# Performance work log

Measured on AMD Instinct MI355X. Metric: run time of the kernel, lower is better.

The kernel has to match this reference:

```python
import jax, jax.numpy as jnp
import numpy as np

B = 16384
WIDE_DIM = 256          # 32 wide features * dim 8
DEEP_DIM = 1024         # 64 deep features * embedding_dim 16
SHARED = [2048, 1024, 512]
DOMAIN = [512, 256]
NUM_DOMAINS = 8


def setup_inputs() -> dict:
    key = jax.random.key(0)
    ks = jax.random.split(key, 20)
    s = 0.01  # embedding_init_var-style small init
    inp = {
        "wide_features": jax.random.normal(ks[0], (B, WIDE_DIM), jnp.float32),
        "deep_features": jax.random.normal(ks[1], (B, DEEP_DIM), jnp.float32),
        "domain_ids": jax.random.randint(ks[2], (B,), 0, NUM_DOMAINS, jnp.int64),
        # shared MLP (weights stored [in, out])
        "W1": jax.random.normal(ks[3], (DEEP_DIM, SHARED[0]), jnp.float32) * s,
        "b1": jnp.zeros((SHARED[0],), jnp.float32),
        "W2": jax.random.normal(ks[4], (SHARED[0], SHARED[1]), jnp.float32) * s,
        "b2": jnp.zeros((SHARED[1],), jnp.float32),
        "W3": jax.random.normal(ks[5], (SHARED[1], SHARED[2]), jnp.float32) * s,
        "b3": jnp.zeros((SHARED[2],), jnp.float32),
        # domain-specific MLP
        "Wd1": jax.random.normal(ks[6], (SHARED[2], DOMAIN[0]), jnp.float32) * s,
        "bd1": jnp.zeros((DOMAIN[0],), jnp.float32),
        "Wd2": jax.random.normal(ks[7], (DOMAIN[0], DOMAIN[1]), jnp.float32) * s,
        "bd2": jnp.zeros((DOMAIN[1],), jnp.float32),
        # per-domain output heads: Linear(DOMAIN[-1], 1) per domain
        "Wh": jax.random.normal(ks[8], (NUM_DOMAINS, DOMAIN[1]), jnp.float32) * s,
        "bh": jnp.zeros((NUM_DOMAINS,), jnp.float32),
    }
    return inp


def reference(wide_features, deep_features, domain_ids,
              W1, b1, W2, b2, W3, b3, Wd1, bd1, Wd2, bd2, Wh, bh):
    # wide part: sum embedding output to a scalar logit per sample [B, 1]
    wide = jnp.sum(wide_features, axis=1, keepdims=True)
    # shared deep MLP
    h = jax.nn.relu(deep_features @ W1 + b1)
    h = jax.nn.relu(h @ W2 + b2)
    shared = jax.nn.relu(h @ W3 + b3)          # [B, 512]
    # domain-specific tower (shared across domains)
    d = jax.nn.relu(shared @ Wd1 + bd1)
    d = jax.nn.relu(d @ Wd2 + bd2)             # [B, 256]
    # per-sample domain head routing: gather head weights, fused dot
    w = Wh[domain_ids]                          # [B, 256]
    head = jnp.sum(d * w, axis=1, keepdims=True) + bh[domain_ids][:, None]  # [B, 1]
    out = jax.nn.sigmoid(wide + head)
    return (out, shared, d)
```

## Files before the change

### kernel.cpp

```cpp
#include <hip/hip_runtime.h>
#include <hip/hip_bf16.h>


typedef __attribute__((ext_vector_type(8))) short short8;
typedef __attribute__((ext_vector_type(4))) float f32x4;

static __device__ __forceinline__ unsigned short f2bf_bits(float x) {
  __hip_bfloat16 h = __float2bfloat16(x);
  return __builtin_bit_cast(unsigned short, h);
}
static __device__ __forceinline__ float bf_bits2f(unsigned short u) {
  __hip_bfloat16 h = __builtin_bit_cast(__hip_bfloat16, u);
  return __bfloat162float(h);
}

static __device__ __forceinline__ void gload16(const void* g, void* l) {
  __builtin_amdgcn_global_load_lds(
      (const __attribute__((address_space(1))) void*)g,
      (__attribute__((address_space(3))) void*)l, 16, 0, 0);
}

static __device__ __forceinline__ unsigned lds_u32(const void* p) {
  return (unsigned)(uintptr_t)(const __attribute__((address_space(3))) void*)p;
}

static __device__ __forceinline__ short8 dsr(unsigned addr) {
  short8 r;
  asm volatile("ds_read_b128 %0, %1" : "=v"(r) : "v"(addr));
  return r;
}

#define MFMA16(a, b, c) __builtin_amdgcn_mfma_f32_16x16x32_bf16((a), (b), (c), 0, 0, 0)
#define SB0() __builtin_amdgcn_sched_barrier(0)
#define PRIO(x) __builtin_amdgcn_s_setprio(x)
#define BAR() __builtin_amdgcn_s_barrier()
#define MEMFENCE() asm volatile("" ::: "memory")

__global__ void transpose_convert(const float* __restrict__ W,
                                  __hip_bfloat16* __restrict__ Wt,
                                  int K, int N) {
  __shared__ float tile[64][65];
  const int k0 = blockIdx.y * 64;
  const int n0 = blockIdx.x * 64;
  const int t  = threadIdx.x;
  const int tn = t & 63;
  const int t4 = t >> 6;
#pragma unroll
  for (int p = 0; p < 16; ++p) {
    int kl = p * 4 + t4;
    tile[kl][tn] = W[(size_t)(k0 + kl) * N + (n0 + tn)];
  }
  __syncthreads();
#pragma unroll
  for (int p = 0; p < 16; ++p) {
    int nl = p * 4 + t4;
    Wt[(size_t)(n0 + nl) * K + (k0 + tn)] = __float2bfloat16(tile[tn][nl]);
  }
}

__global__ void f32_to_bf16(const float* __restrict__ in,
                            unsigned short* __restrict__ out, int n8) {
  int i = blockIdx.x * blockDim.x + threadIdx.x;
  if (i >= n8) return;
  const f32x4* p = (const f32x4*)in + (size_t)i * 2;
  f32x4 a = p[0], b = p[1];
  short8 o;
  o[0] = (short)f2bf_bits(a[0]); o[1] = (short)f2bf_bits(a[1]);
  o[2] = (short)f2bf_bits(a[2]); o[3] = (short)f2bf_bits(a[3]);
  o[4] = (short)f2bf_bits(b[0]); o[5] = (short)f2bf_bits(b[1]);
  o[6] = (short)f2bf_bits(b[2]); o[7] = (short)f2bf_bits(b[3]);
  *(short8*)(out + (size_t)i * 8) = o;
}

__global__ __launch_bounds__(512, 2) void gemm_2c(
    const __hip_bfloat16* __restrict__ A,
    const __hip_bfloat16* __restrict__ Bt,
    const float* __restrict__ bias,
    __hip_bfloat16* __restrict__ Cb,
    float* __restrict__ Cf,
    int N, int K, int nbx) {
  __shared__ char lds[131072];

  const int tid  = threadIdx.x;
  const int lane = tid & 63;
  const int wid  = tid >> 6;
  const int wm   = wid >> 2;
  const int wn   = wid & 3;

  const int nwg = gridDim.x;
  const int cpx = nwg >> 3;
  const int id  = blockIdx.x;
  const int swz = (id & 7) * cpx + (id >> 3);
  const int bm  = (swz / nbx) * 256;
  const int bn  = (swz % nbx) * 256;

  const int ln15 = lane & 15;
  const unsigned cswz = (unsigned)((((lane >> 4) ^ (lane & 7)) << 4));

  const unsigned aoff = (unsigned)((wm * 128 + ln15) * 128) + cswz;
  const unsigned boff = 32768u + (unsigned)((wn * 64 + ln15) * 128) + cswz;

  const int nt = K >> 6;

  const __hip_bfloat16* baseA = A  + (size_t)(bm + (tid >> 3)) * K +
                                ((tid & 7) ^ ((tid >> 3) & 7)) * 8;
  const __hip_bfloat16* baseB = Bt + (size_t)(bn + (tid >> 3)) * K +
                                ((tid & 7) ^ ((tid >> 3) & 7)) * 8;
  const unsigned ldst0 = (unsigned)(wid * 1024);

  auto stage = [&](int kt, int half, int isB) {
    const __hip_bfloat16* base = isB ? baseB : baseA;
    char* dst = lds + ((kt & 1) * 65536) + (isB ? 32768 : 0) + half * 16384;
#pragma unroll
    for (int q = 0; q < 2; ++q) {
      gload16(base + (size_t)((half * 128 + q * 64) * K + kt * 64),
              dst + q * 8192 + ldst0);
    }
  };

  auto LD = [&](unsigned off) -> short8 {
    return *(const short8*)&lds[off];
  };

  f32x4 acc[8][4] = {};
  short8 aLo[4][2], aHi[4][2], b0v[2][2], b1v[2][2];

  stage(0, 0, 1); stage(0, 1, 1); stage(0, 0, 0); stage(0, 1, 0);
  if (nt > 1) {
    stage(1, 0, 1); stage(1, 1, 1); stage(1, 0, 0); stage(1, 1, 0);
    asm volatile("s_waitcnt vmcnt(8)");
  } else {
    asm volatile("s_waitcnt vmcnt(0)");
  }
  BAR();
  MEMFENCE();
#pragma unroll
  for (int mi = 0; mi < 4; ++mi)
#pragma unroll
    for (int kk = 0; kk < 2; ++kk)
      aLo[mi][kk] = LD((aoff + (unsigned)(mi * 2048)) ^ (unsigned)(kk << 6));
#pragma unroll
  for (int nj = 0; nj < 2; ++nj)
#pragma unroll
    for (int kk = 0; kk < 2; ++kk)
      b0v[nj][kk] = LD((boff + (unsigned)(nj * 2048)) ^ (unsigned)(kk << 6));

  for (int t = 0; t < nt; ++t) {
    const unsigned po = (unsigned)(t & 1) * 65536u;
    const unsigned pn = po ^ 65536u;

#pragma unroll
    for (int nj = 0; nj < 2; ++nj)
#pragma unroll
      for (int kk = 0; kk < 2; ++kk)
        b1v[nj][kk] = LD((po + boff + (unsigned)((nj + 2) * 2048)) ^ (unsigned)(kk << 6));
    PRIO(1);
#pragma unroll
    for (int kk = 0; kk < 2; ++kk)
#pragma unroll
      for (int mi = 0; mi < 4; ++mi)
#pragma unroll
        for (int nj = 0; nj < 2; ++nj)
          acc[mi][nj] = MFMA16(aLo[mi][kk], b0v[nj][kk], acc[mi][nj]);
    PRIO(0);

#pragma unroll
    for (int mi = 0; mi < 4; ++mi)
#pragma unroll
      for (int kk = 0; kk < 2; ++kk)
        aHi[mi][kk] = LD((po + aoff + (unsigned)((mi + 4) * 2048)) ^ (unsigned)(kk << 6));
    PRIO(1);
#pragma unroll
    for (int kk = 0; kk < 2; ++kk)
#pragma unroll
      for (int mi = 0; mi < 4; ++mi)
#pragma unroll
        for (int nj = 0; nj < 2; ++nj)
          acc[mi][nj + 2] = MFMA16(aLo[mi][kk], b1v[nj][kk], acc[mi][nj + 2]);
    PRIO(0);
    BAR();
    MEMFENCE();

    PRIO(1);
#pragma unroll
    for (int kk = 0; kk < 2; ++kk)
#pragma unroll
      for (int mi = 0; mi < 4; ++mi)
#pragma unroll
        for (int nj = 0; nj < 2; ++nj)
          acc[mi + 4][nj] = MFMA16(aHi[mi][kk], b0v[nj][kk], acc[mi + 4][nj]);
    PRIO(0);
    if (t + 2 < nt) { stage(t + 2, 0, 1); stage(t + 2, 1, 1); }
    if (t + 1 < nt) {
      if (t + 2 < nt) asm volatile("s_waitcnt vmcnt(4)");
      else            asm volatile("s_waitcnt vmcnt(0)");
      BAR();
      MEMFENCE();
    }

    if (t + 1 < nt) {
#pragma unroll
      for (int mi = 0; mi < 4; ++mi)
#pragma unroll
        for (int kk = 0; kk < 2; ++kk)
          aLo[mi][kk] = LD((pn + aoff + (unsigned)(mi * 2048)) ^ (unsigned)(kk << 6));
#pragma unroll
      for (int nj = 0; nj < 2; ++nj)
#pragma unroll
        for (int kk = 0; kk < 2; ++kk)
          b0v[nj][kk] = LD((pn + boff + (unsigned)(nj * 2048)) ^ (unsigned)(kk << 6));
    }
    PRIO(1);
#pragma unroll
    for (int kk = 0; kk < 2; ++kk)
#pragma unroll
      for (int mi = 0; mi < 4; ++mi)
#pragma unroll
        for (int nj = 0; nj < 2; ++nj)
          acc[mi + 4][nj + 2] = MFMA16(aHi[mi][kk], b1v[nj][kk], acc[mi + 4][nj + 2]);
    PRIO(0);
    if (t + 2 < nt) { stage(t + 2, 0, 0); stage(t + 2, 1, 0); }
  }

  float biasv[4];
#pragma unroll
  for (int nj = 0; nj < 4; ++nj)
    biasv[nj] = bias[bn + wn * 64 + nj * 16 + ln15];

#pragma unroll
  for (int mi = 0; mi < 8; ++mi) {
    int row0 = bm + wm * 128 + mi * 16 + (lane >> 4) * 4;
#pragma unroll
    for (int nj = 0; nj < 4; ++nj) {
      int col = bn + wn * 64 + nj * 16 + ln15;
#pragma unroll
      for (int r = 0; r < 4; ++r) {
        float v = acc[mi][nj][r] + biasv[nj];
        v = v > 0.f ? v : 0.f;
        size_t idx = (size_t)(row0 + r) * N + col;
        Cb[idx] = __float2bfloat16(v);
        if (Cf) Cf[idx] = v;
      }
    }
  }
}

__global__ __launch_bounds__(512, 2) void gemm_128(
    const __hip_bfloat16* __restrict__ A,
    const __hip_bfloat16* __restrict__ Bt,
    const float* __restrict__ bias,
    __hip_bfloat16* __restrict__ Cb,
    float* __restrict__ Cf,
    int N, int K, int nbx) {
  __shared__ char lds[98304];

  const int tid  = threadIdx.x;
  const int lane = tid & 63;
  const int wid  = tid >> 6;
  const int wm   = wid >> 2;
  const int wn   = wid & 3;

  const int nwg = gridDim.x;
  const int cpx = nwg >> 3;
  const int id  = blockIdx.x;
  const int swz = (id & 7) * cpx + (id >> 3);
  const int bm  = (swz / nbx) * 128;
  const int bn  = (swz % nbx) * 256;

  const int ln15 = lane & 15;
  const unsigned cswz = (unsigned)((((lane >> 4) ^ (lane & 7)) << 4));

  const unsigned lbase = lds_u32(lds);
  const unsigned arow0 = lbase + (unsigned)(wm * 64 + ln15) * 128u + cswz;
  const unsigned brow0 = lbase + 16384u + (unsigned)(wn * 64 + ln15) * 128u + cswz;

  const int nt = K >> 6;

  const int swc = (tid & 7) ^ ((tid >> 3) & 7);
  const __hip_bfloat16* baseA = A  + (size_t)(bm + (tid >> 3)) * K + swc * 8;
  const __hip_bfloat16* baseB = Bt + (size_t)(bn + (tid >> 3)) * K + swc * 8;
  const unsigned ldst0 = (unsigned)(tid * 16);

  auto stageA = [&](int kt, int half) {
    char* dst = lds + ((kt & 1) * 49152) + half * 8192;
    gload16(baseA + (size_t)((half * 64) * K + kt * 64), dst + ldst0);
  };
  auto stageB = [&](int kt, int half) {
    char* dst = lds + ((kt & 1) * 49152) + 16384 + half * 16384;
#pragma unroll
    for (int q = 0; q < 2; ++q) {
      gload16(baseB + (size_t)((half * 128 + q * 64) * K + kt * 64),
              dst + q * 8192 + ldst0);
    }
  };

  f32x4 acc[4][4] = {};
  short8 aLo[2][2], aHi[2][2], b0v[2][2], b1v[2][2];

  stageB(0, 0); stageB(0, 1); stageA(0, 0); stageA(0, 1);
  if (nt > 1) {
    stageB(1, 0); stageB(1, 1); stageA(1, 0); stageA(1, 1);
    asm volatile("s_waitcnt vmcnt(6)");
  } else {
    asm volatile("s_waitcnt vmcnt(0)");
  }
  BAR();
#pragma unroll
  for (int mi = 0; mi < 2; ++mi) {
    unsigned ad = arow0 + (unsigned)(mi * 2048);
    aLo[mi][0] = dsr(ad); aLo[mi][1] = dsr(ad ^ 64u);
  }

  for (int t = 0; t < nt; ++t) {
    const unsigned po = (unsigned)(t & 1) * 49152u;
    const unsigned pn = po ^ 49152u;

    asm volatile("s_waitcnt lgkmcnt(0)");
    SB0();
#pragma unroll
    for (int nj = 0; nj < 2; ++nj) b0v[nj][0] = dsr(brow0 + po + (unsigned)(nj * 2048));
#pragma unroll
    for (int nj = 0; nj < 2; ++nj) b0v[nj][1] = dsr((brow0 + po + (unsigned)(nj * 2048)) ^ 64u);
#pragma unroll
    for (int nj = 0; nj < 2; ++nj) b1v[nj][0] = dsr(brow0 + po + (unsigned)((nj + 2) * 2048));
#pragma unroll
    for (int nj = 0; nj < 2; ++nj) b1v[nj][1] = dsr((brow0 + po + (unsigned)((nj + 2) * 2048)) ^ 64u);
    asm volatile("s_waitcnt lgkmcnt(6)");
    SB0();
    PRIO(1);
#pragma unroll
    for (int mi = 0; mi < 2; ++mi)
#pragma unroll
      for (int nj = 0; nj < 2; ++nj)
        acc[mi][nj] = MFMA16(aLo[mi][0], b0v[nj][0], acc[mi][nj]);
    asm volatile("s_waitcnt lgkmcnt(4)");
    SB0();
#pragma unroll
    for (int mi = 0; mi < 2; ++mi)
#pragma unroll
      for (int nj = 0; nj < 2; ++nj)
        acc[mi][nj] = MFMA16(aLo[mi][1], b0v[nj][1], acc[mi][nj]);
    PRIO(0);

#pragma unroll
    for (int mi = 0; mi < 2; ++mi) {
      unsigned ad = arow0 + po + (unsigned)((mi + 2) * 2048);
      aHi[mi][0] = dsr(ad); aHi[mi][1] = dsr(ad ^ 64u);
    }
    asm volatile("s_waitcnt lgkmcnt(4)");
    SB0();
    PRIO(1);
#pragma unroll
    for (int kk = 0; kk < 2; ++kk)
#pragma unroll
      for (int mi = 0; mi < 2; ++mi)
#pragma unroll
        for (int nj = 0; nj < 2; ++nj)
          acc[mi][nj + 2] = MFMA16(aLo[mi][kk], b1v[nj][kk], acc[mi][nj + 2]);
    PRIO(0);
    BAR();

    asm volatile("s_waitcnt lgkmcnt(0)");
    SB0();
    PRIO(1);
#pragma unroll
    for (int kk = 0; kk < 2; ++kk)
#pragma unroll
      for (int mi = 0; mi < 2; ++mi)
#pragma unroll
        for (int nj = 0; nj < 2; ++nj)
          acc[mi + 2][nj] = MFMA16(aHi[mi][kk], b0v[nj][kk], acc[mi + 2][nj]);
    PRIO(0);
    if (t + 2 < nt) { stageB(t + 2, 0); stageB(t + 2, 1); }
    if (t + 1 < nt) {
      if (t + 2 < nt) asm volatile("s_waitcnt vmcnt(4)");
      else            asm volatile("s_waitcnt vmcnt(0)");
      BAR();
    }

    if (t + 1 < nt) {
#pragma unroll
      for (int mi = 0; mi < 2; ++mi) {
        unsigned ad = arow0 + pn + (unsigned)(mi * 2048);
        aLo[mi][0] = dsr(ad); aLo[mi][1] = dsr(ad ^ 64u);
      }
    }
    SB0();
    PRIO(1);
#pragma unroll
    for (int kk = 0; kk < 2; ++kk)
#pragma unroll
      for (int mi = 0; mi < 2; ++mi)
#pragma unroll
        for (int nj = 0; nj < 2; ++nj)
          acc[mi + 2][nj + 2] = MFMA16(aHi[mi][kk], b1v[nj][kk], acc[mi + 2][nj + 2]);
    PRIO(0);
    if (t + 2 < nt) { stageA(t + 2, 0); stageA(t + 2, 1); }
  }

  float biasv[4];
#pragma unroll
  for (int nj = 0; nj < 4; ++nj)
    biasv[nj] = bias[bn + wn * 64 + nj * 16 + ln15];

#pragma unroll
  for (int mi = 0; mi < 4; ++mi) {
    int row0 = bm + wm * 64 + mi * 16 + (lane >> 4) * 4;
#pragma unroll
    for (int nj = 0; nj < 4; ++nj) {
      int col = bn + wn * 64 + nj * 16 + ln15;
#pragma unroll
      for (int r = 0; r < 4; ++r) {
        float v = acc[mi][nj][r] + biasv[nj];
        v = v > 0.f ? v : 0.f;
        size_t idx = (size_t)(row0 + r) * N + col;
        Cb[idx] = __float2bfloat16(v);
        if (Cf) Cf[idx] = v;
      }
    }
  }
}

__global__ __launch_bounds__(512, 2) void gemm_l5h(
    const __hip_bfloat16* __restrict__ A,
    const __hip_bfloat16* __restrict__ Bt,
    const float* __restrict__ bias,
    float* __restrict__ Df,
    const float* __restrict__ wide,
    const int* __restrict__ dom,
    const float* __restrict__ Wh,
    const float* __restrict__ bh,
    float* __restrict__ outp,
    int K) {
  __shared__ char lds[98304];

  const int tid  = threadIdx.x;
  const int lane = tid & 63;
  const int wid  = tid >> 6;
  const int wm   = wid >> 2;
  const int wn   = wid & 3;

  const int nwg = gridDim.x;
  const int cpx = nwg >> 3;
  const int id  = blockIdx.x;
  const int swz = (id & 7) * cpx + (id >> 3);
  const int bm  = swz * 128;

  const int ln15 = lane & 15;
  const unsigned cswz = (unsigned)((((lane >> 4) ^ (lane & 7)) << 4));

  const unsigned lbase = lds_u32(lds);
  const unsigned arow0 = lbase + (unsigned)(wm * 64 + ln15) * 128u + cswz;
  const unsigned brow0 = lbase + 16384u + (unsigned)(wn * 64 + ln15) * 128u + cswz;

  const int nt = K >> 6;

  const int swc = (tid & 7) ^ ((tid >> 3) & 7);
  const __hip_bfloat16* baseA = A  + (size_t)(bm + (tid >> 3)) * K + swc * 8;
  const __hip_bfloat16* baseB = Bt + (size_t)(tid >> 3) * K + swc * 8;
  const unsigned ldst0 = (unsigned)(tid * 16);

  auto stageA = [&](int kt, int half) {
    char* dst = lds + ((kt & 1) * 49152) + half * 8192;
    gload16(baseA + (size_t)((half * 64) * K + kt * 64), dst + ldst0);
  };
  auto stageB = [&](int kt, int half) {
    char* dst = lds + ((kt & 1) * 49152) + 16384 + half * 16384;
#pragma unroll
    for (int q = 0; q < 2; ++q) {
      gload16(baseB + (size_t)((half * 128 + q * 64) * K + kt * 64),
              dst + q * 8192 + ldst0);
    }
  };

  f32x4 acc[4][4] = {};
  short8 aLo[2][2], aHi[2][2], b0v[2][2], b1v[2][2];

  stageB(0, 0); stageB(0, 1); stageA(0, 0); stageA(0, 1);
  if (nt > 1) {
    stageB(1, 0); stageB(1, 1); stageA(1, 0); stageA(1, 1);
    asm volatile("s_waitcnt vmcnt(6)");
  } else {
    asm volatile("s_waitcnt vmcnt(0)");
  }
  BAR();
#pragma unroll
  for (int mi = 0; mi < 2; ++mi) {
    unsigned ad = arow0 + (unsigned)(mi * 2048);
    aLo[mi][0] = dsr(ad); aLo[mi][1] = dsr(ad ^ 64u);
  }

  for (int t = 0; t < nt; ++t) {
    const unsigned po = (unsigned)(t & 1) * 49152u;
    const unsigned pn = po ^ 49152u;

    asm volatile("s_waitcnt lgkmcnt(0)");
    SB0();
#pragma unroll
    for (int nj = 0; nj < 2; ++nj) b0v[nj][0] = dsr(brow0 + po + (unsigned)(nj * 2048));
#pragma unroll
    for (int nj = 0; nj < 2; ++nj) b0v[nj][1] = dsr((brow0 + po + (unsigned)(nj * 2048)) ^ 64u);
#pragma unroll
    for (int nj = 0; nj < 2; ++nj) b1v[nj][0] = dsr(brow0 + po + (unsigned)((nj + 2) * 2048));
#pragma unroll
    for (int nj = 0; nj < 2; ++nj) b1v[nj][1] = dsr((brow0 + po + (unsigned)((nj + 2) * 2048)) ^ 64u);
    asm volatile("s_waitcnt lgkmcnt(6)");
    SB0();
    PRIO(1);
#pragma unroll
    for (int mi = 0; mi < 2; ++mi)
#pragma unroll
      for (int nj = 0; nj < 2; ++nj)
        acc[mi][nj] = MFMA16(aLo[mi][0], b0v[nj][0], acc[mi][nj]);
    asm volatile("s_waitcnt lgkmcnt(4)");
    SB0();
#pragma unroll
    for (int mi = 0; mi < 2; ++mi)
#pragma unroll
      for (int nj = 0; nj < 2; ++nj)
        acc[mi][nj] = MFMA16(aLo[mi][1], b0v[nj][1], acc[mi][nj]);
    PRIO(0);

#pragma unroll
    for (int mi = 0; mi < 2; ++mi) {
      unsigned ad = arow0 + po + (unsigned)((mi + 2) * 2048);
      aHi[mi][0] = dsr(ad); aHi[mi][1] = dsr(ad ^ 64u);
    }
    asm volatile("s_waitcnt lgkmcnt(4)");
    SB0();
    PRIO(1);
#pragma unroll
    for (int kk = 0; kk < 2; ++kk)
#pragma unroll
      for (int mi = 0; mi < 2; ++mi)
#pragma unroll
        for (int nj = 0; nj < 2; ++nj)
          acc[mi][nj + 2] = MFMA16(aLo[mi][kk], b1v[nj][kk], acc[mi][nj + 2]);
    PRIO(0);
    BAR();

    asm volatile("s_waitcnt lgkmcnt(0)");
    SB0();
    PRIO(1);
#pragma unroll
    for (int kk = 0; kk < 2; ++kk)
#pragma unroll
      for (int mi = 0; mi < 2; ++mi)
#pragma unroll
        for (int nj = 0; nj < 2; ++nj)
          acc[mi + 2][nj] = MFMA16(aHi[mi][kk], b0v[nj][kk], acc[mi + 2][nj]);
    PRIO(0);
    if (t + 2 < nt) { stageB(t + 2, 0); stageB(t + 2, 1); }
    if (t + 1 < nt) {
      if (t + 2 < nt) asm volatile("s_waitcnt vmcnt(4)");
      else            asm volatile("s_waitcnt vmcnt(0)");
      BAR();
    }

    if (t + 1 < nt) {
#pragma unroll
      for (int mi = 0; mi < 2; ++mi) {
        unsigned ad = arow0 + pn + (unsigned)(mi * 2048);
        aLo[mi][0] = dsr(ad); aLo[mi][1] = dsr(ad ^ 64u);
      }
    }
    SB0();
    PRIO(1);
#pragma unroll
    for (int kk = 0; kk < 2; ++kk)
#pragma unroll
      for (int mi = 0; mi < 2; ++mi)
#pragma unroll
        for (int nj = 0; nj < 2; ++nj)
          acc[mi + 2][nj + 2] = MFMA16(aHi[mi][kk], b1v[nj][kk], acc[mi + 2][nj + 2]);
    PRIO(0);
    if (t + 2 < nt) { stageA(t + 2, 0); stageA(t + 2, 1); }
  }

  BAR();
  MEMFENCE();
  unsigned short* ldsD = (unsigned short*)lds;
  float* ldsH = (float*)(lds + 128 * 264 * 2);

  float biasv[4];
#pragma unroll
  for (int nj = 0; nj < 4; ++nj)
    biasv[nj] = bias[wn * 64 + nj * 16 + ln15];

#pragma unroll
  for (int mi = 0; mi < 4; ++mi) {
    int lrow0 = wm * 64 + mi * 16 + (lane >> 4) * 4;
#pragma unroll
    for (int nj = 0; nj < 4; ++nj) {
      int col = wn * 64 + nj * 16 + ln15;
#pragma unroll
      for (int r = 0; r < 4; ++r) {
        float v = acc[mi][nj][r] + biasv[nj];
        v = v > 0.f ? v : 0.f;
        Df[(size_t)(bm + lrow0 + r) * 256 + col] = v;
        ldsD[(lrow0 + r) * 264 + col] = f2bf_bits(v);
      }
    }
  }

  const int erow = tid >> 2;
  const int eq   = tid & 3;
  float s = 0.f;
  {
    const f32x4* wp = (const f32x4*)(wide + (size_t)(bm + erow) * 256 + eq * 64);
#pragma unroll
    for (int j = 0; j < 16; ++j) {
      f32x4 w = wp[j];
      s += w[0] + w[1] + w[2] + w[3];
    }
  }
  BAR();
  MEMFENCE();

  const int dm = dom[bm + erow];
  float h = 0.f;
  {
    const f32x4* hp = (const f32x4*)(Wh + (size_t)dm * 256 + eq * 64);
    const short8* dp = (const short8*)(ldsD + erow * 264 + eq * 64);
#pragma unroll
    for (int j = 0; j < 8; ++j) {
      short8 d8 = dp[j];
      f32x4 h0 = hp[j * 2], h1 = hp[j * 2 + 1];
      h += bf_bits2f((unsigned short)d8[0]) * h0[0] +
           bf_bits2f((unsigned short)d8[1]) * h0[1] +
           bf_bits2f((unsigned short)d8[2]) * h0[2] +
           bf_bits2f((unsigned short)d8[3]) * h0[3] +
           bf_bits2f((unsigned short)d8[4]) * h1[0] +
           bf_bits2f((unsigned short)d8[5]) * h1[1] +
           bf_bits2f((unsigned short)d8[6]) * h1[2] +
           bf_bits2f((unsigned short)d8[7]) * h1[3];
    }
  }
  ldsH[erow * 4 + eq] = s + h;
  BAR();
  MEMFENCE();

  if (tid < 128) {
    float val = ldsH[tid * 4] + ldsH[tid * 4 + 1] +
                ldsH[tid * 4 + 2] + ldsH[tid * 4 + 3];
    int dmr = dom[bm + tid];
    float x = val + bh[dmr];
    outp[bm + tid] = 1.f / (1.f + __expf(-x));
  }
}

extern "C" void kernel_launch(void* const* d_in, const int* in_sizes, int n_in,
                              void* d_out, int out_size, void* d_ws, size_t ws_size,
                              hipStream_t stream) {
  const float* wide = (const float*)d_in[0];
  const float* deep = (const float*)d_in[1];
  const int*   dom  = (const int*)d_in[2];
  const float* W1  = (const float*)d_in[3];
  const float* b1  = (const float*)d_in[4];
  const float* W2  = (const float*)d_in[5];
  const float* b2  = (const float*)d_in[6];
  const float* W3  = (const float*)d_in[7];
  const float* b3  = (const float*)d_in[8];
  const float* Wd1 = (const float*)d_in[9];
  const float* bd1 = (const float*)d_in[10];
  const float* Wd2 = (const float*)d_in[11];
  const float* bd2 = (const float*)d_in[12];
  const float* Wh  = (const float*)d_in[13];
  const float* bh  = (const float*)d_in[14];
  float* out = (float*)d_out;

  const int B = 16384;
  char* ws = (char*)d_ws;
  __hip_bfloat16* buf0 = (__hip_bfloat16*)ws;
  __hip_bfloat16* buf1 = (__hip_bfloat16*)(ws + 33554432ull);
  __hip_bfloat16* W1t  = (__hip_bfloat16*)(ws + 100663296ull);
  __hip_bfloat16* W2t  = W1t + 2048 * 1024;
  __hip_bfloat16* W3t  = W2t + 1024 * 2048;
  __hip_bfloat16* Wd1t = W3t + 512 * 1024;
  __hip_bfloat16* Wd2t = Wd1t + 512 * 512;

  transpose_convert<<<dim3(2048 / 64, 1024 / 64), 256, 0, stream>>>(W1, W1t, 1024, 2048);
  transpose_convert<<<dim3(1024 / 64, 2048 / 64), 256, 0, stream>>>(W2, W2t, 2048, 1024);
  transpose_convert<<<dim3(512 / 64, 1024 / 64), 256, 0, stream>>>(W3, W3t, 1024, 512);
  transpose_convert<<<dim3(512 / 64, 512 / 64), 256, 0, stream>>>(Wd1, Wd1t, 512, 512);
  transpose_convert<<<dim3(256 / 64, 512 / 64), 256, 0, stream>>>(Wd2, Wd2t, 512, 256);

  {
    int n8 = B * 1024 / 8;
    f32_to_bf16<<<(n8 + 255) / 256, 256, 0, stream>>>(deep, (unsigned short*)buf0, n8);
  }

  float* shared_out = out + B;
  float* d_out_f    = out + B + (size_t)B * 512;

  gemm_2c<<<dim3((2048 / 256) * (B / 256)), 512, 0, stream>>>(
      buf0, W1t, b1, buf1, nullptr, 2048, 1024, 2048 / 256);
  gemm_2c<<<dim3((1024 / 256) * (B / 256)), 512, 0, stream>>>(
      buf1, W2t, b2, buf0, nullptr, 1024, 2048, 1024 / 256);
  gemm_128<<<dim3((B / 128) * (512 / 256)), 512, 0, stream>>>(
      buf0, W3t, b3, buf1, shared_out, 512, 1024, 512 / 256);
  gemm_128<<<dim3((B / 128) * (512 / 256)), 512, 0, stream>>>(
      buf1, Wd1t, bd1, buf0, nullptr, 512, 512, 512 / 256);
  gemm_l5h<<<dim3(B / 128), 512, 0, stream>>>(
      buf0, Wd2t, bd2, d_out_f, wide, dom, Wh, bh, out, 512);
}
```

Before: 218.9 us.

## Fuse prep kernels into one launch and use 32x32 MFMA GEMM for layer 2

Merges the five weight transpose-convert launches and the input f32-to-bf16 conversion into a single prep kernel that dispatches work by block index, removing five launch overheads and the gaps between them. Adds gemm_2c32, a variant of the 256x256 double-buffered GEMM that uses 32x32x16 bf16 MFMA with a matching LDS swizzle and epilogue, and uses it for the second shared layer. The larger MFMA shape cuts LDS reads per FLOP but changes the register footprint and the output write pattern.

```diff
diff --git a/kernel.cpp b/kernel.cpp
--- a/kernel.cpp
+++ b/kernel.cpp
@@ -4,6 +4,7 @@
 
 typedef __attribute__((ext_vector_type(8))) short short8;
 typedef __attribute__((ext_vector_type(4))) float f32x4;
+typedef __attribute__((ext_vector_type(16))) float f32x16;
 
 static __device__ __forceinline__ unsigned short f2bf_bits(float x) {
   __hip_bfloat16 h = __float2bfloat16(x);
@@ -31,17 +32,43 @@
 }
 
 #define MFMA16(a, b, c) __builtin_amdgcn_mfma_f32_16x16x32_bf16((a), (b), (c), 0, 0, 0)
+#define MFMA32(a, b, c) __builtin_amdgcn_mfma_f32_32x32x16_bf16((a), (b), (c), 0, 0, 0)
 #define SB0() __builtin_amdgcn_sched_barrier(0)
 #define PRIO(x) __builtin_amdgcn_s_setprio(x)
 #define BAR() __builtin_amdgcn_s_barrier()
 #define MEMFENCE() asm volatile("" ::: "memory")
 
-__global__ void transpose_convert(const float* __restrict__ W,
-                                  __hip_bfloat16* __restrict__ Wt,
-                                  int K, int N) {
+__global__ __launch_bounds__(256) void prep(
+    const float* __restrict__ deep, unsigned short* __restrict__ deepb,
+    const float* __restrict__ W1, __hip_bfloat16* __restrict__ W1t,
+    const float* __restrict__ W2, __hip_bfloat16* __restrict__ W2t,
+    const float* __restrict__ W3, __hip_bfloat16* __restrict__ W3t,
+    const float* __restrict__ Wd1, __hip_bfloat16* __restrict__ Wd1t,
+    const float* __restrict__ Wd2, __hip_bfloat16* __restrict__ Wd2t) {
   __shared__ float tile[64][65];
-  const int k0 = blockIdx.y * 64;
-  const int n0 = blockIdx.x * 64;
+  int blk = blockIdx.x;
+  if (blk < 8192) {
+    int i = blk * 256 + threadIdx.x;
+    const f32x4* p = (const f32x4*)deep + (size_t)i * 2;
+    f32x4 a = p[0], b = p[1];
+    short8 o;
+    o[0] = (short)f2bf_bits(a[0]); o[1] = (short)f2bf_bits(a[1]);
+    o[2] = (short)f2bf_bits(a[2]); o[3] = (short)f2bf_bits(a[3]);
+    o[4] = (short)f2bf_bits(b[0]); o[5] = (short)f2bf_bits(b[1]);
+    o[6] = (short)f2bf_bits(b[2]); o[7] = (short)f2bf_bits(b[3]);
+    *(short8*)(deepb + (size_t)i * 8) = o;
+    return;
+  }
+  blk -= 8192;
+  const float* W; __hip_bfloat16* Wt; int K, N;
+  if (blk < 512)       {             W = W1;  Wt = W1t;  K = 1024; N = 2048; }
+  else if (blk < 1024) { blk -= 512;  W = W2;  Wt = W2t;  K = 2048; N = 1024; }
+  else if (blk < 1152) { blk -= 1024; W = W3;  Wt = W3t;  K = 1024; N = 512; }
+  else if (blk < 1216) { blk -= 1152; W = Wd1; Wt = Wd1t; K = 512;  N = 512; }
+  else                 { blk -= 1216; W = Wd2; Wt = Wd2t; K = 512;  N = 256; }
+  const int ntx = N >> 6;
+  const int k0 = (blk / ntx) * 64;
+  const int n0 = (blk % ntx) * 64;
   const int t  = threadIdx.x;
   const int tn = t & 63;
   const int t4 = t >> 6;
@@ -56,20 +83,6 @@
     int nl = p * 4 + t4;
     Wt[(size_t)(n0 + nl) * K + (k0 + tn)] = __float2bfloat16(tile[tn][nl]);
   }
-}
-
-__global__ void f32_to_bf16(const float* __restrict__ in,
-                            unsigned short* __restrict__ out, int n8) {
-  int i = blockIdx.x * blockDim.x + threadIdx.x;
-  if (i >= n8) return;
-  const f32x4* p = (const f32x4*)in + (size_t)i * 2;
-  f32x4 a = p[0], b = p[1];
-  short8 o;
-  o[0] = (short)f2bf_bits(a[0]); o[1] = (short)f2bf_bits(a[1]);
-  o[2] = (short)f2bf_bits(a[2]); o[3] = (short)f2bf_bits(a[3]);
-  o[4] = (short)f2bf_bits(b[0]); o[5] = (short)f2bf_bits(b[1]);
-  o[6] = (short)f2bf_bits(b[2]); o[7] = (short)f2bf_bits(b[3]);
-  *(short8*)(out + (size_t)i * 8) = o;
 }
 
 __global__ __launch_bounds__(512, 2) void gemm_2c(
@@ -238,6 +251,166 @@
         float v = acc[mi][nj][r] + biasv[nj];
         v = v > 0.f ? v : 0.f;
         size_t idx = (size_t)(row0 + r) * N + col;
+        Cb[idx] = __float2bfloat16(v);
+        if (Cf) Cf[idx] = v;
+      }
+    }
+  }
+}
+
+__global__ __launch_bounds__(512, 2) void gemm_2c32(
+    const __hip_bfloat16* __restrict__ A,
+    const __hip_bfloat16* __restrict__ Bt,
+    const float* __restrict__ bias,
+    __hip_bfloat16* __restrict__ Cb,
+    float* __restrict__ Cf,
+    int N, int K, int nbx) {
+  __shared__ char lds[131072];
+
+  const int tid  = threadIdx.x;
+  const int lane = tid & 63;
+  const int wid  = tid >> 6;
+  const int wm   = wid >> 2;
+  const int wn   = wid & 3;
+
+  const int nwg = gridDim.x;
+  const int cpx = nwg >> 3;
+  const int id  = blockIdx.x;
+  const int swz = (id & 7) * cpx + (id >> 3);
+  const int bm  = (swz / nbx) * 256;
+  const int bn  = (swz % nbx) * 256;
+
+  const int ln31 = lane & 31;
+  const unsigned cs32 = (unsigned)((((lane >> 5) ^ (lane & 7)) << 4));
+
+  const unsigned aoff = (unsigned)((wm * 128 + ln31) * 128) + cs32;
+  const unsigned boff = 32768u + (unsigned)((wn * 64 + ln31) * 128) + cs32;
+
+  const int nt = K >> 6;
+
+  const __hip_bfloat16* baseA = A  + (size_t)(bm + (tid >> 3)) * K +
+                                ((tid & 7) ^ ((tid >> 3) & 7)) * 8;
+  const __hip_bfloat16* baseB = Bt + (size_t)(bn + (tid >> 3)) * K +
+                                ((tid & 7) ^ ((tid >> 3) & 7)) * 8;
+  const unsigned ldst0 = (unsigned)(wid * 1024);
+
+  auto stage = [&](int kt, int half, int isB) {
+    const __hip_bfloat16* base = isB ? baseB : baseA;
+    char* dst = lds + ((kt & 1) * 65536) + (isB ? 32768 : 0) + half * 16384;
+#pragma unroll
+    for (int q = 0; q < 2; ++q) {
+      gload16(base + (size_t)((half * 128 + q * 64) * K + kt * 64),
+              dst + q * 8192 + ldst0);
+    }
+  };
+
+  auto LD = [&](unsigned off) -> short8 {
+    return *(const short8*)&lds[off];
+  };
+
+  f32x16 acc[4][2] = {};
+  short8 aLo[2][4], aHi[2][4], b0v[4], b1v[4];
+
+  stage(0, 0, 1); stage(0, 1, 1); stage(0, 0, 0); stage(0, 1, 0);
+  if (nt > 1) {
+    stage(1, 0, 1); stage(1, 1, 1); stage(1, 0, 0); stage(1, 1, 0);
+    asm volatile("s_waitcnt vmcnt(8)");
+  } else {
+    asm volatile("s_waitcnt vmcnt(0)");
+  }
+  BAR();
+  MEMFENCE();
+#pragma unroll
+  for (int mf = 0; mf < 2; ++mf)
+#pragma unroll
+    for (int ks = 0; ks < 4; ++ks)
+      aLo[mf][ks] = LD((aoff + (unsigned)(mf * 4096)) ^ (unsigned)(ks << 5));
+#pragma unroll
+  for (int ks = 0; ks < 4; ++ks)
+    b0v[ks] = LD(boff ^ (unsigned)(ks << 5));
+
+  for (int t = 0; t < nt; ++t) {
+    const unsigned po = (unsigned)(t & 1) * 65536u;
+    const unsigned pn = po ^ 65536u;
+
+#pragma unroll
+    for (int ks = 0; ks < 4; ++ks)
+      b1v[ks] = LD((po + boff + 4096u) ^ (unsigned)(ks << 5));
+    PRIO(1);
+#pragma unroll
+    for (int ks = 0; ks < 4; ++ks)
+#pragma unroll
+      for (int mf = 0; mf < 2; ++mf)
+        acc[mf][0] = MFMA32(aLo[mf][ks], b0v[ks], acc[mf][0]);
+    PRIO(0);
+
+#pragma unroll
+    for (int mf = 0; mf < 2; ++mf)
+#pragma unroll
+      for (int ks = 0; ks < 4; ++ks)
+        aHi[mf][ks] = LD((po + aoff + (unsigned)((mf + 2) * 4096)) ^ (unsigned)(ks << 5));
+    PRIO(1);
+#pragma unroll
+    for (int ks = 0; ks < 4; ++ks)
+#pragma unroll
+      for (int mf = 0; mf < 2; ++mf)
+        acc[mf][1] = MFMA32(aLo[mf][ks], b1v[ks], acc[mf][1]);
+    PRIO(0);
+    BAR();
+    MEMFENCE();
+
+    PRIO(1);
+#pragma unroll
+    for (int ks = 0; ks < 4; ++ks)
+#pragma unroll
+      for (int mf = 0; mf < 2; ++mf)
+        acc[mf + 2][0] = MFMA32(aHi[mf][ks], b0v[ks], acc[mf + 2][0]);
+    PRIO(0);
+    if (t + 2 < nt) { stage(t + 2, 0, 1); stage(t + 2, 1, 1); }
+    if (t + 1 < nt) {
+      if (t + 2 < nt) asm volatile("s_waitcnt vmcnt(4)");
+      else            asm volatile("s_waitcnt vmcnt(0)");
+      BAR();
+      MEMFENCE();
+    }
+
+    if (t + 1 < nt) {
+#pragma unroll
+      for (int mf = 0; mf < 2; ++mf)
+#pragma unroll
+        for (int ks = 0; ks < 4; ++ks)
+          aLo[mf][ks] = LD((pn + aoff + (unsigned)(mf * 4096)) ^ (unsigned)(ks << 5));
+#pragma unroll
+      for (int ks = 0; ks < 4; ++ks)
+        b0v[ks] = LD((pn + boff) ^ (unsigned)(ks << 5));
+    }
+    PRIO(1);
+#pragma unroll
+    for (int ks = 0; ks < 4; ++ks)
+#pragma unroll
+      for (int mf = 0; mf < 2; ++mf)
+        acc[mf + 2][1] = MFMA32(aHi[mf][ks], b1v[ks], acc[mf + 2][1]);
+    PRIO(0);
+    if (t + 2 < nt) { stage(t + 2, 0, 0); stage(t + 2, 1, 0); }
+  }
+
+  float biasv[2];
+#pragma unroll
+  for (int nf = 0; nf < 2; ++nf)
+    biasv[nf] = bias[bn + wn * 64 + nf * 32 + ln31];
+
+#pragma unroll
+  for (int mf = 0; mf < 4; ++mf) {
+    int rbase = bm + wm * 128 + mf * 32 + 4 * (lane >> 5);
+#pragma unroll
+    for (int nf = 0; nf < 2; ++nf) {
+      int col = bn + wn * 64 + nf * 32 + ln31;
+#pragma unroll
+      for (int r = 0; r < 16; ++r) {
+        int row = rbase + (r & 3) + 8 * (r >> 2);
+        float v = acc[mf][nf][r] + biasv[nf];
+        v = v > 0.f ? v : 0.f;
+        size_t idx = (size_t)row * N + col;
         Cb[idx] = __float2bfloat16(v);
         if (Cf) Cf[idx] = v;
       }
@@ -679,23 +852,15 @@
   __hip_bfloat16* Wd1t = W3t + 512 * 1024;
   __hip_bfloat16* Wd2t = Wd1t + 512 * 512;
 
-  transpose_convert<<<dim3(2048 / 64, 1024 / 64), 256, 0, stream>>>(W1, W1t, 1024, 2048);
-  transpose_convert<<<dim3(1024 / 64, 2048 / 64), 256, 0, stream>>>(W2, W2t, 2048, 1024);
-  transpose_convert<<<dim3(512 / 64, 1024 / 64), 256, 0, stream>>>(W3, W3t, 1024, 512);
-  transpose_convert<<<dim3(512 / 64, 512 / 64), 256, 0, stream>>>(Wd1, Wd1t, 512, 512);
-  transpose_convert<<<dim3(256 / 64, 512 / 64), 256, 0, stream>>>(Wd2, Wd2t, 512, 256);
-
-  {
-    int n8 = B * 1024 / 8;
-    f32_to_bf16<<<(n8 + 255) / 256, 256, 0, stream>>>(deep, (unsigned short*)buf0, n8);
-  }
+  prep<<<dim3(8192 + 1248), 256, 0, stream>>>(
+      deep, (unsigned short*)buf0, W1, W1t, W2, W2t, W3, W3t, Wd1, Wd1t, Wd2, Wd2t);
 
   float* shared_out = out + B;
   float* d_out_f    = out + B + (size_t)B * 512;
 
   gemm_2c<<<dim3((2048 / 256) * (B / 256)), 512, 0, stream>>>(
       buf0, W1t, b1, buf1, nullptr, 2048, 1024, 2048 / 256);
-  gemm_2c<<<dim3((1024 / 256) * (B / 256)), 512, 0, stream>>>(
+  gemm_2c32<<<dim3((1024 / 256) * (B / 256)), 512, 0, stream>>>(
       buf1, W2t, b2, buf0, nullptr, 1024, 2048, 1024 / 256);
   gemm_128<<<dim3((B / 128) * (512 / 256)), 512, 0, stream>>>(
       buf0, W3t, b3, buf1, shared_out, 512, 1024, 512 / 256);
```

Measured after the change: 218.1 us. About the same (-0.4%).
